# Kernel optimization log

Hardware: AMD Instinct MI355X
Metric: run time of the kernel (lower is better)

Reference implementation:

```python
import jax, jax.numpy as jnp
import numpy as np

NUM_TOKENS = 128
STRING_SIZE = 512
HIDDEN_SIZE = 2048
L_IN = 256
L_OUT = 256
MAX_PROGRAM_LENGTH = 10


def _lstm_scan(xs, h, c, Wih, Whh, b):
    """Run a PyTorch-convention LSTM (gate order i,f,g,o) over xs [L, D]."""
    def step(carry, x):
        h, c = carry
        g = x @ Wih.T + h @ Whh.T + b          # [4H]
        i, f, gg, o = jnp.split(g, 4)
        c2 = jax.nn.sigmoid(f) * c + jax.nn.sigmoid(i) * jnp.tanh(gg)
        h2 = jax.nn.sigmoid(o) * jnp.tanh(c2)
        return (h2, c2), None
    (h, c), _ = jax.lax.scan(step, (h, c), xs)
    return h, c


def setup_inputs() -> dict:
    key = jax.random.key(0)
    ks = jax.random.split(key, 13)
    H, S = HIDDEN_SIZE, STRING_SIZE
    def p(k, shape, scale=0.02):
        return scale * jax.random.normal(k, shape, dtype=jnp.float32)
    return {
        "input_sequence": jax.random.randint(ks[0], (L_IN,), 0, NUM_TOKENS),
        "output_sequence": jax.random.randint(ks[1], (L_OUT,), 0, NUM_TOKENS),
        "embed": p(ks[2], (NUM_TOKENS, S), 1.0),
        "eos": p(ks[3], (S,), 1.0),
        "in_Wih": p(ks[4], (4 * H, S)), "in_Whh": p(ks[5], (4 * H, H)), "in_b": p(ks[6], (4 * H,)),
        "out_Wih": p(ks[7], (4 * H, S)), "out_Whh": p(ks[8], (4 * H, H)), "out_b": p(ks[9], (4 * H,)),
        "prog_Wih": p(ks[10], (4 * H, H)), "prog_Whh": p(ks[11], (4 * H, H)), "prog_b": p(ks[12], (4 * H,)),
    }


def reference(input_sequence, output_sequence, embed, eos,
              in_Wih, in_Whh, in_b, out_Wih, out_Whh, out_b,
              prog_Wih, prog_Whh, prog_b):
    H = in_Whh.shape[1]
    h = jnp.zeros((H,), embed.dtype)
    c = jnp.zeros((H,), embed.dtype)
    # encode input string (+ end-of-sequence token) with input_lstm
    xs_in = jnp.concatenate([embed[input_sequence], eos[None]], axis=0)   # [L_in+1, S]
    h, c = _lstm_scan(xs_in, h, c, in_Wih, in_Whh, in_b)
    # encode output string (+ eos) with output_lstm, state carried over
    xs_out = jnp.concatenate([embed[output_sequence], eos[None]], axis=0)  # [L_out+1, S]
    h, c = _lstm_scan(xs_out, h, c, out_Wih, out_Whh, out_b)
    def prog_step(carry, _):
        h, c = carry
        g = h @ prog_Wih.T + h @ prog_Whh.T + prog_b
        i, f, gg, o = jnp.split(g, 4)
        c2 = jax.nn.sigmoid(f) * c + jax.nn.sigmoid(i) * jnp.tanh(gg)
        h2 = jax.nn.sigmoid(o) * jnp.tanh(c2)
        return (h2, c2), h2
    _, prog = jax.lax.scan(prog_step, (h, c), None, length=MAX_PROGRAM_LENGTH)
    return prog  # [MAX_PROGRAM_LENGTH, H] (stack of program hidden states)
```

## Files before the change

kernel.cpp:

```cpp
#include <hip/hip_runtime.h>

typedef unsigned short u16;
typedef unsigned int u32;
typedef unsigned long long u64;

#define NBLK 256

__device__ __forceinline__ float b2f(u16 u) {
    u32 i = ((u32)u) << 16;
    return __builtin_bit_cast(float, i);
}
__device__ __forceinline__ u16 f2b(float f) {
    u32 b = __builtin_bit_cast(u32, f);
    b += 0x7FFFu + ((b >> 16) & 1u);
    return (u16)(b >> 16);
}
__device__ __forceinline__ float sigm(float x) {
    return 1.f / (1.f + __expf(-x));
}
__device__ __forceinline__ float tanh_fast(float x) {
    float a = fabsf(x);
    float e = __expf(-2.f * a);
    float r = (1.f - e) / (1.f + e);
    return copysignf(r, x);
}

__global__ void __launch_bounds__(256)
xproj_kernel(const float* __restrict__ embed, const float* __restrict__ eos,
             const int* __restrict__ seq, const float* __restrict__ W,
             const float* __restrict__ bias, float* __restrict__ Xp)
{
    __shared__ float xs[8][512];
    const int tid = threadIdx.x;
    const int t0 = blockIdx.y * 8;
    const int nt = min(8, 257 - t0);

    for (int idx = tid; idx < nt * 512; idx += 256) {
        int tt = idx >> 9, col = idx & 511;
        int t = t0 + tt;
        xs[tt][col] = (t < 256) ? embed[(size_t)seq[t] * 512 + col] : eos[col];
    }
    __syncthreads();

    const int lane = tid & 63;
    const int wv = tid >> 6;

    float xr[8][8];
#pragma unroll
    for (int tt = 0; tt < 8; ++tt) {
        *(float4*)&xr[tt][0] = *(const float4*)&xs[tt][lane * 8];
        *(float4*)&xr[tt][4] = *(const float4*)&xs[tt][lane * 8 + 4];
    }

#pragma unroll 1
    for (int rr = 0; rr < 8; ++rr) {
        int r = blockIdx.x * 32 + wv * 8 + rr;
        float wf[8];
        *(float4*)&wf[0] = *(const float4*)&W[(size_t)r * 512 + lane * 8];
        *(float4*)&wf[4] = *(const float4*)&W[(size_t)r * 512 + lane * 8 + 4];
        float acc[8];
#pragma unroll
        for (int tt = 0; tt < 8; tt++) {
            float a = 0.f;
#pragma unroll
            for (int j = 0; j < 8; j++) a = fmaf(wf[j], xr[tt][j], a);
            acc[tt] = a;
        }
#pragma unroll
        for (int tt = 0; tt < 8; tt++) {
            float a = acc[tt];
#pragma unroll
            for (int off = 32; off > 0; off >>= 1) a += __shfl_xor(a, off, 64);
            if (lane == 0 && tt < nt) {
                int g = r >> 11, rem = r & 2047, wgi = rem >> 3, j = rem & 7;
                Xp[(size_t)(t0 + tt) * 8192 + (wgi << 5) + (g << 3) + j] = a + bias[r];
            }
        }
    }
}

__global__ void __launch_bounds__(512, 1)
rnn_coop(const float* __restrict__ WhhA, const float* __restrict__ WhhB,
         const float* __restrict__ pWih, const float* __restrict__ pWhh,
         const float* __restrict__ pB,
         const float* __restrict__ Xp0, const float* __restrict__ Xp1,
         u32* __restrict__ hseqB, float* __restrict__ out)
{
    __shared__ __align__(16) float hs[2048];
    __shared__ float gsum[32];

    const int wg = blockIdx.x;
    const int tid = threadIdx.x;
    const int lane = tid & 63;
    const int wv = tid >> 6;

    float w[4][32];
    float c_reg = 0.f;

    if (tid < 32) gsum[tid] = 0.f;

    float xp_cur = 0.f, xp_nxt = 0.f;
    if (wv == 0 && lane < 32)
        xp_cur = Xp0[(size_t)0 * 8192 + (wg << 5) + lane];

    for (int t = 0; t < 524; ++t) {
        const int phase = (t < 257) ? 0 : (t < 514) ? 1 : 2;

        if (t == 0 || t == 257 || t == 514) {
            if (phase < 2) {
                const float* Ws = phase ? WhhB : WhhA;
#pragma unroll
                for (int rr = 0; rr < 4; ++rr) {
                    int rl = (wv << 2) + rr;
                    const float* Wr = Ws + (size_t)(((rl >> 3) << 11) + (wg << 3) + (rl & 7)) * 2048;
#pragma unroll
                    for (int q = 0; q < 8; ++q)
                        *(float4*)&w[rr][q * 4] = *(const float4*)&Wr[(q << 8) + (lane << 2)];
                }
            } else {
#pragma unroll
                for (int rr = 0; rr < 4; ++rr) {
                    int rl = (wv << 2) + rr;
                    size_t off = (size_t)(((rl >> 3) << 11) + (wg << 3) + (rl & 7)) * 2048;
#pragma unroll
                    for (int q = 0; q < 8; ++q) {
                        float4 a = *(const float4*)&pWih[off + (q << 8) + (lane << 2)];
                        float4 b = *(const float4*)&pWhh[off + (q << 8) + (lane << 2)];
                        float4 s;
                        s.x = a.x + b.x; s.y = a.y + b.y;
                        s.z = a.z + b.z; s.w = a.w + b.w;
                        *(float4*)&w[rr][q * 4] = s;
                    }
                }
            }
        }

        if (t > 0) {
            const u64* src = (const u64*)hseqB + (size_t)(t - 1) * 512 + tid;
            u64 a = __hip_atomic_load(src, __ATOMIC_RELAXED, __HIP_MEMORY_SCOPE_AGENT);
            while ((u16)a == 0xFFFFu || (u16)(a >> 16) == 0xFFFFu ||
                   (u16)(a >> 32) == 0xFFFFu || (u16)(a >> 48) == 0xFFFFu) {
                __builtin_amdgcn_s_sleep(1);
                a = __hip_atomic_load(src, __ATOMIC_RELAXED, __HIP_MEMORY_SCOPE_AGENT);
            }
            float4 hv;
            hv.x = b2f((u16)a);         hv.y = b2f((u16)(a >> 16));
            hv.z = b2f((u16)(a >> 32)); hv.w = b2f((u16)(a >> 48));
            *(float4*)&hs[tid << 2] = hv;
        }
        __syncthreads();

        if (wv == 0 && lane < 32 && t < 523) {
            const int tn = t + 1;
            if (tn < 257)       xp_nxt = Xp0[(size_t)tn * 8192 + (wg << 5) + lane];
            else if (tn < 514)  xp_nxt = Xp1[(size_t)(tn - 257) * 8192 + (wg << 5) + lane];
            else                xp_nxt = pB[((lane >> 3) << 11) + (wg << 3) + (lane & 7)];
        }

        if (t > 0) {
            float a0 = 0.f, a1 = 0.f, a2 = 0.f, a3 = 0.f;
#pragma unroll
            for (int q = 0; q < 8; ++q) {
                float4 hv = *(const float4*)&hs[(q << 8) + (lane << 2)];
#pragma unroll
                for (int j = 0; j < 4; ++j) {
                    float h = ((const float*)&hv)[j];
                    a0 = fmaf(w[0][q * 4 + j], h, a0);
                    a1 = fmaf(w[1][q * 4 + j], h, a1);
                    a2 = fmaf(w[2][q * 4 + j], h, a2);
                    a3 = fmaf(w[3][q * 4 + j], h, a3);
                }
            }
#pragma unroll
            for (int off = 32; off > 0; off >>= 1) {
                a0 += __shfl_xor(a0, off, 64);
                a1 += __shfl_xor(a1, off, 64);
                a2 += __shfl_xor(a2, off, 64);
                a3 += __shfl_xor(a3, off, 64);
            }
            if (lane == 0) {
                const int rl = wv << 2;
                gsum[rl]     = a0;
                gsum[rl + 1] = a1;
                gsum[rl + 2] = a2;
                gsum[rl + 3] = a3;
            }
        }
        __syncthreads();

        if (wv == 0) {
            float tot = xp_cur + gsum[lane & 31];
            float act = ((lane >> 3) == 2) ? tanh_fast(tot) : sigm(tot);
            const int j = lane & 7;
            float fi = __shfl(act, j, 64);
            float ff = __shfl(act, 8 + j, 64);
            float fg = __shfl(act, 16 + j, 64);
            float fo = __shfl(act, 24 + j, 64);
            c_reg = ff * c_reg + fi * fg;
            float h2 = fo * tanh_fast(c_reg);
            u32 hb = (u32)f2b(h2);
            u32 lo = (u32)__shfl((int)hb, (lane & 3) * 2, 64);
            u32 hi = (u32)__shfl((int)hb, (lane & 3) * 2 + 1, 64);
            if (lane < 4)
                __hip_atomic_store(&hseqB[(size_t)t * 1024 + (wg << 2) + lane],
                                   (hi << 16) | lo,
                                   __ATOMIC_RELAXED, __HIP_MEMORY_SCOPE_AGENT);
            if (phase == 2 && lane < 8)
                out[(size_t)(t - 514) * 2048 + (wg << 3) + lane] = h2;
        }
        xp_cur = xp_nxt;
    }
}

extern "C" void kernel_launch(void* const* d_in, const int* in_sizes, int n_in,
                              void* d_out, int out_size, void* d_ws, size_t ws_size,
                              hipStream_t stream) {
    const int*   in_seq   = (const int*)d_in[0];
    const int*   out_seq  = (const int*)d_in[1];
    const float* embed    = (const float*)d_in[2];
    const float* eos      = (const float*)d_in[3];
    const float* in_Wih   = (const float*)d_in[4];
    const float* in_Whh   = (const float*)d_in[5];
    const float* in_b     = (const float*)d_in[6];
    const float* out_Wih  = (const float*)d_in[7];
    const float* out_Whh  = (const float*)d_in[8];
    const float* out_b    = (const float*)d_in[9];
    const float* pg_Wih   = (const float*)d_in[10];
    const float* pg_Whh   = (const float*)d_in[11];
    const float* pg_b     = (const float*)d_in[12];

    float* Xp0   = (float*)d_ws;
    float* Xp1   = Xp0 + (size_t)257 * 8192;
    u32*   hseqB = (u32*)(Xp1 + (size_t)257 * 8192);

    hipMemsetAsync(hseqB, 0xFF, (size_t)524 * 1024 * sizeof(u32), stream);

    dim3 g1(256, 33), b1(256);
    hipLaunchKernelGGL(xproj_kernel, g1, b1, 0, stream, embed, eos, in_seq,  in_Wih,  in_b,  Xp0);
    hipLaunchKernelGGL(xproj_kernel, g1, b1, 0, stream, embed, eos, out_seq, out_Wih, out_b, Xp1);

    float* out = (float*)d_out;
    void* args[] = { (void*)&in_Whh, (void*)&out_Whh, (void*)&pg_Wih, (void*)&pg_Whh,
                     (void*)&pg_b, (void*)&Xp0, (void*)&Xp1, (void*)&hseqB, (void*)&out };
    hipLaunchCooperativeKernel((const void*)rnn_coop, dim3(NBLK), dim3(512),
                               args, 0, stream);
}
```

Before: 1.984 ms.

## Fuse input projection into recurrent cooperative kernel with shared-memory Wih and lookahead ring

Removes the two separate xproj kernels and their global Xp buffers. Each workgroup now keeps its 32 rows of the input and output Wih in LDS and computes the input projection four steps ahead into a small ring buffer, so this work sits inside otherwise idle time in the serial recurrence. The token embedding for upcoming steps is prefetched into a double buffer. The s_sleep in the spin-wait is also removed, which should cut wake-up latency at the cost of more polling traffic. In exchange, each step adds extra LDS work and uses about 140KB of LDS per block.

New measurement: 2.274 ms. +14.6%, slower.

```diff
diff --git a/kernel.cpp b/kernel.cpp
--- a/kernel.cpp
+++ b/kernel.cpp
@@ -25,69 +25,22 @@
     return copysignf(r, x);
 }
 
-__global__ void __launch_bounds__(256)
-xproj_kernel(const float* __restrict__ embed, const float* __restrict__ eos,
-             const int* __restrict__ seq, const float* __restrict__ W,
-             const float* __restrict__ bias, float* __restrict__ Xp)
-{
-    __shared__ float xs[8][512];
-    const int tid = threadIdx.x;
-    const int t0 = blockIdx.y * 8;
-    const int nt = min(8, 257 - t0);
-
-    for (int idx = tid; idx < nt * 512; idx += 256) {
-        int tt = idx >> 9, col = idx & 511;
-        int t = t0 + tt;
-        xs[tt][col] = (t < 256) ? embed[(size_t)seq[t] * 512 + col] : eos[col];
-    }
-    __syncthreads();
-
-    const int lane = tid & 63;
-    const int wv = tid >> 6;
-
-    float xr[8][8];
-#pragma unroll
-    for (int tt = 0; tt < 8; ++tt) {
-        *(float4*)&xr[tt][0] = *(const float4*)&xs[tt][lane * 8];
-        *(float4*)&xr[tt][4] = *(const float4*)&xs[tt][lane * 8 + 4];
-    }
-
-#pragma unroll 1
-    for (int rr = 0; rr < 8; ++rr) {
-        int r = blockIdx.x * 32 + wv * 8 + rr;
-        float wf[8];
-        *(float4*)&wf[0] = *(const float4*)&W[(size_t)r * 512 + lane * 8];
-        *(float4*)&wf[4] = *(const float4*)&W[(size_t)r * 512 + lane * 8 + 4];
-        float acc[8];
-#pragma unroll
-        for (int tt = 0; tt < 8; tt++) {
-            float a = 0.f;
-#pragma unroll
-            for (int j = 0; j < 8; j++) a = fmaf(wf[j], xr[tt][j], a);
-            acc[tt] = a;
-        }
-#pragma unroll
-        for (int tt = 0; tt < 8; tt++) {
-            float a = acc[tt];
-#pragma unroll
-            for (int off = 32; off > 0; off >>= 1) a += __shfl_xor(a, off, 64);
-            if (lane == 0 && tt < nt) {
-                int g = r >> 11, rem = r & 2047, wgi = rem >> 3, j = rem & 7;
-                Xp[(size_t)(t0 + tt) * 8192 + (wgi << 5) + (g << 3) + j] = a + bias[r];
-            }
-        }
-    }
-}
-
 __global__ void __launch_bounds__(512, 1)
 rnn_coop(const float* __restrict__ WhhA, const float* __restrict__ WhhB,
          const float* __restrict__ pWih, const float* __restrict__ pWhh,
          const float* __restrict__ pB,
-         const float* __restrict__ Xp0, const float* __restrict__ Xp1,
+         const float* __restrict__ inWih, const float* __restrict__ outWih,
+         const float* __restrict__ in_b, const float* __restrict__ out_b,
+         const float* __restrict__ embed, const float* __restrict__ eos,
+         const int* __restrict__ in_seq, const int* __restrict__ out_seq,
          u32* __restrict__ hseqB, float* __restrict__ out)
 {
+    __shared__ __align__(16) float wihA[32 * 512];
+    __shared__ __align__(16) float wihB[32 * 512];
     __shared__ __align__(16) float hs[2048];
-    __shared__ float gsum[32];
+    __shared__ __align__(16) float xbuf[2][512];
+    __shared__ float ring[8][32];
+    __shared__ float biasA[32], biasB[32], gsum[32];
 
     const int wg = blockIdx.x;
     const int tid = threadIdx.x;
@@ -96,12 +49,57 @@
 
     float w[4][32];
     float c_reg = 0.f;
-
-    if (tid < 32) gsum[tid] = 0.f;
-
-    float xp_cur = 0.f, xp_nxt = 0.f;
-    if (wv == 0 && lane < 32)
-        xp_cur = Xp0[(size_t)0 * 8192 + (wg << 5) + lane];
+    float xp2 = 0.f;
+
+    for (int idx = tid; idx < 4096; idx += 512) {
+        int m = idx >> 7, c4 = (idx & 127) << 2;
+        size_t grow = (size_t)(((m >> 3) << 11) + (wg << 3) + (m & 7)) * 512;
+        *(float4*)&wihA[m * 512 + c4] = *(const float4*)&inWih[grow + c4];
+        *(float4*)&wihB[m * 512 + c4] = *(const float4*)&outWih[grow + c4];
+    }
+    if (tid < 32) {
+        int gofs = ((tid >> 3) << 11) + (wg << 3) + (tid & 7);
+        biasA[tid] = in_b[gofs];
+        biasB[tid] = out_b[gofs];
+        gsum[tid] = 0.f;
+    }
+    __syncthreads();
+
+    for (int tt = 0; tt < 4; ++tt) {
+        xbuf[0][tid] = embed[(size_t)in_seq[tt] * 512 + tid];
+        __syncthreads();
+        float a0 = 0.f, a1 = 0.f, a2 = 0.f, a3 = 0.f;
+        const int m0 = wv << 2;
+#pragma unroll
+        for (int q = 0; q < 2; ++q) {
+            float4 xv = *(const float4*)&xbuf[0][(q << 8) + (lane << 2)];
+            float4 w0 = *(const float4*)&wihA[(m0 + 0) * 512 + (q << 8) + (lane << 2)];
+            float4 w1 = *(const float4*)&wihA[(m0 + 1) * 512 + (q << 8) + (lane << 2)];
+            float4 w2 = *(const float4*)&wihA[(m0 + 2) * 512 + (q << 8) + (lane << 2)];
+            float4 w3 = *(const float4*)&wihA[(m0 + 3) * 512 + (q << 8) + (lane << 2)];
+            a0 = fmaf(w0.x, xv.x, fmaf(w0.y, xv.y, fmaf(w0.z, xv.z, fmaf(w0.w, xv.w, a0))));
+            a1 = fmaf(w1.x, xv.x, fmaf(w1.y, xv.y, fmaf(w1.z, xv.z, fmaf(w1.w, xv.w, a1))));
+            a2 = fmaf(w2.x, xv.x, fmaf(w2.y, xv.y, fmaf(w2.z, xv.z, fmaf(w2.w, xv.w, a2))));
+            a3 = fmaf(w3.x, xv.x, fmaf(w3.y, xv.y, fmaf(w3.z, xv.z, fmaf(w3.w, xv.w, a3))));
+        }
+#pragma unroll
+        for (int off = 32; off > 0; off >>= 1) {
+            a0 += __shfl_xor(a0, off, 64);
+            a1 += __shfl_xor(a1, off, 64);
+            a2 += __shfl_xor(a2, off, 64);
+            a3 += __shfl_xor(a3, off, 64);
+        }
+        if (lane == 0) {
+            ring[tt][m0]     = a0 + biasA[m0];
+            ring[tt][m0 + 1] = a1 + biasA[m0 + 1];
+            ring[tt][m0 + 2] = a2 + biasA[m0 + 2];
+            ring[tt][m0 + 3] = a3 + biasA[m0 + 3];
+        }
+        __syncthreads();
+    }
+    xbuf[0][tid] = embed[(size_t)in_seq[4] * 512 + tid];
+    int tok_cur = in_seq[5];
+    __syncthreads();
 
     for (int t = 0; t < 524; ++t) {
         const int phase = (t < 257) ? 0 : (t < 514) ? 1 : 2;
@@ -132,6 +130,8 @@
                         *(float4*)&w[rr][q * 4] = s;
                     }
                 }
+                if (wv == 0 && lane < 32)
+                    xp2 = pB[((lane >> 3) << 11) + (wg << 3) + (lane & 7)];
             }
         }
 
@@ -139,10 +139,8 @@
             const u64* src = (const u64*)hseqB + (size_t)(t - 1) * 512 + tid;
             u64 a = __hip_atomic_load(src, __ATOMIC_RELAXED, __HIP_MEMORY_SCOPE_AGENT);
             while ((u16)a == 0xFFFFu || (u16)(a >> 16) == 0xFFFFu ||
-                   (u16)(a >> 32) == 0xFFFFu || (u16)(a >> 48) == 0xFFFFu) {
-                __builtin_amdgcn_s_sleep(1);
+                   (u16)(a >> 32) == 0xFFFFu || (u16)(a >> 48) == 0xFFFFu)
                 a = __hip_atomic_load(src, __ATOMIC_RELAXED, __HIP_MEMORY_SCOPE_AGENT);
-            }
             float4 hv;
             hv.x = b2f((u16)a);         hv.y = b2f((u16)(a >> 16));
             hv.z = b2f((u16)(a >> 32)); hv.w = b2f((u16)(a >> 48));
@@ -150,12 +148,14 @@
         }
         __syncthreads();
 
-        if (wv == 0 && lane < 32 && t < 523) {
-            const int tn = t + 1;
-            if (tn < 257)       xp_nxt = Xp0[(size_t)tn * 8192 + (wg << 5) + lane];
-            else if (tn < 514)  xp_nxt = Xp1[(size_t)(tn - 257) * 8192 + (wg << 5) + lane];
-            else                xp_nxt = pB[((lane >> 3) << 11) + (wg << 3) + (lane & 7)];
-        }
+        const int idx1 = t + 5, idx2 = t + 6;
+        int tok_nxt = -2;
+        float xnext = 0.f;
+        if (idx2 <= 513)
+            tok_nxt = (idx2 < 257) ? ((idx2 < 256) ? in_seq[idx2] : -1)
+                                   : ((idx2 < 513) ? out_seq[idx2 - 257] : -1);
+        if (idx1 <= 513)
+            xnext = (tok_cur < 0) ? eos[tid] : embed[(size_t)tok_cur * 512 + tid];
 
         if (t > 0) {
             float a0 = 0.f, a1 = 0.f, a2 = 0.f, a3 = 0.f;
@@ -189,7 +189,8 @@
         __syncthreads();
 
         if (wv == 0) {
-            float tot = xp_cur + gsum[lane & 31];
+            float xpv = (phase < 2) ? ring[t & 7][lane & 31] : xp2;
+            float tot = xpv + gsum[lane & 31];
             float act = ((lane >> 3) == 2) ? tanh_fast(tot) : sigm(tot);
             const int j = lane & 7;
             float fi = __shfl(act, j, 64);
@@ -208,7 +209,43 @@
             if (phase == 2 && lane < 8)
                 out[(size_t)(t - 514) * 2048 + (wg << 3) + lane] = h2;
         }
-        xp_cur = xp_nxt;
+
+        const int tt = t + 4;
+        if (tt <= 513) {
+            const bool inph = tt < 257;
+            const float* wih = inph ? wihA : wihB;
+            const float* bl  = inph ? biasA : biasB;
+            const float* xb  = xbuf[tt & 1];
+            float a0 = 0.f, a1 = 0.f, a2 = 0.f, a3 = 0.f;
+            const int m0 = wv << 2;
+#pragma unroll
+            for (int q = 0; q < 2; ++q) {
+                float4 xv = *(const float4*)&xb[(q << 8) + (lane << 2)];
+                float4 w0 = *(const float4*)&wih[(m0 + 0) * 512 + (q << 8) + (lane << 2)];
+                float4 w1 = *(const float4*)&wih[(m0 + 1) * 512 + (q << 8) + (lane << 2)];
+                float4 w2 = *(const float4*)&wih[(m0 + 2) * 512 + (q << 8) + (lane << 2)];
+                float4 w3 = *(const float4*)&wih[(m0 + 3) * 512 + (q << 8) + (lane << 2)];
+                a0 = fmaf(w0.x, xv.x, fmaf(w0.y, xv.y, fmaf(w0.z, xv.z, fmaf(w0.w, xv.w, a0))));
+                a1 = fmaf(w1.x, xv.x, fmaf(w1.y, xv.y, fmaf(w1.z, xv.z, fmaf(w1.w, xv.w, a1))));
+                a2 = fmaf(w2.x, xv.x, fmaf(w2.y, xv.y, fmaf(w2.z, xv.z, fmaf(w2.w, xv.w, a2))));
+                a3 = fmaf(w3.x, xv.x, fmaf(w3.y, xv.y, fmaf(w3.z, xv.z, fmaf(w3.w, xv.w, a3))));
+            }
+#pragma unroll
+            for (int off = 32; off > 0; off >>= 1) {
+                a0 += __shfl_xor(a0, off, 64);
+                a1 += __shfl_xor(a1, off, 64);
+                a2 += __shfl_xor(a2, off, 64);
+                a3 += __shfl_xor(a3, off, 64);
+            }
+            if (lane == 0) {
+                ring[tt & 7][m0]     = a0 + bl[m0];
+                ring[tt & 7][m0 + 1] = a1 + bl[m0 + 1];
+                ring[tt & 7][m0 + 2] = a2 + bl[m0 + 2];
+                ring[tt & 7][m0 + 3] = a3 + bl[m0 + 3];
+            }
+        }
+        if (idx1 <= 513) xbuf[idx1 & 1][tid] = xnext;
+        tok_cur = tok_nxt;
     }
 }
 
@@ -229,19 +266,16 @@
     const float* pg_Whh   = (const float*)d_in[11];
     const float* pg_b     = (const float*)d_in[12];
 
-    float* Xp0   = (float*)d_ws;
-    float* Xp1   = Xp0 + (size_t)257 * 8192;
-    u32*   hseqB = (u32*)(Xp1 + (size_t)257 * 8192);
+    u32* hseqB = (u32*)d_ws;
 
     hipMemsetAsync(hseqB, 0xFF, (size_t)524 * 1024 * sizeof(u32), stream);
-
-    dim3 g1(256, 33), b1(256);
-    hipLaunchKernelGGL(xproj_kernel, g1, b1, 0, stream, embed, eos, in_seq,  in_Wih,  in_b,  Xp0);
-    hipLaunchKernelGGL(xproj_kernel, g1, b1, 0, stream, embed, eos, out_seq, out_Wih, out_b, Xp1);
 
     float* out = (float*)d_out;
     void* args[] = { (void*)&in_Whh, (void*)&out_Whh, (void*)&pg_Wih, (void*)&pg_Whh,
-                     (void*)&pg_b, (void*)&Xp0, (void*)&Xp1, (void*)&hseqB, (void*)&out };
+                     (void*)&pg_b,
+                     (void*)&in_Wih, (void*)&out_Wih, (void*)&in_b, (void*)&out_b,
+                     (void*)&embed, (void*)&eos, (void*)&in_seq, (void*)&out_seq,
+                     (void*)&hseqB, (void*)&out };
     hipLaunchCooperativeKernel((const void*)rnn_coop, dim3(NBLK), dim3(512),
                                args, 0, stream);
 }
```

## Merge input projections into one launch with weights held in registers

Applied to the files above, without the earlier changes.

The two xproj launches become a single 512-block launch, with blockIdx selecting the input or output LSTM. Each block now loads its 32 weight rows once into registers and loops over all 33 timestep groups, instead of re-reading weights for each (row, group) block. Shuffle reductions are batched across 8 rows to gain ILP. The cost is fewer blocks (512 versus 2×8448) and more registers per thread, which may lower occupancy. The recurrent kernel that dominates total time is unchanged.

Result: no change. 1.968 ms (-0.8%).

```diff
diff --git a/kernel.cpp b/kernel.cpp
--- a/kernel.cpp
+++ b/kernel.cpp
@@ -27,55 +27,73 @@
 
 __global__ void __launch_bounds__(256)
 xproj_kernel(const float* __restrict__ embed, const float* __restrict__ eos,
-             const int* __restrict__ seq, const float* __restrict__ W,
-             const float* __restrict__ bias, float* __restrict__ Xp)
+             const int* __restrict__ seqA, const int* __restrict__ seqB,
+             const float* __restrict__ WA, const float* __restrict__ WB,
+             const float* __restrict__ bA, const float* __restrict__ bB,
+             float* __restrict__ XpA, float* __restrict__ XpB)
 {
-    __shared__ float xs[8][512];
+    __shared__ __align__(16) float xs[8][512];
+    const int which = blockIdx.x >> 8;
+    const int bx = blockIdx.x & 255;
+    const int* __restrict__ seq  = which ? seqB : seqA;
+    const float* __restrict__ W  = which ? WB : WA;
+    const float* __restrict__ bias = which ? bB : bA;
+    float* __restrict__ Xp = which ? XpB : XpA;
+
     const int tid = threadIdx.x;
-    const int t0 = blockIdx.y * 8;
-    const int nt = min(8, 257 - t0);
-
-    for (int idx = tid; idx < nt * 512; idx += 256) {
-        int tt = idx >> 9, col = idx & 511;
-        int t = t0 + tt;
-        xs[tt][col] = (t < 256) ? embed[(size_t)seq[t] * 512 + col] : eos[col];
-    }
-    __syncthreads();
-
     const int lane = tid & 63;
     const int wv = tid >> 6;
 
-    float xr[8][8];
-#pragma unroll
-    for (int tt = 0; tt < 8; ++tt) {
-        *(float4*)&xr[tt][0] = *(const float4*)&xs[tt][lane * 8];
-        *(float4*)&xr[tt][4] = *(const float4*)&xs[tt][lane * 8 + 4];
+    float w[8][8];
+    float breg[8];
+    int slot[8];
+#pragma unroll
+    for (int rr = 0; rr < 8; ++rr) {
+        const int r = bx * 32 + wv * 8 + rr;
+        *(float4*)&w[rr][0] = *(const float4*)&W[(size_t)r * 512 + (lane << 2)];
+        *(float4*)&w[rr][4] = *(const float4*)&W[(size_t)r * 512 + 256 + (lane << 2)];
+        breg[rr] = bias[r];
+        int g = r >> 11, rem = r & 2047;
+        slot[rr] = ((rem >> 3) << 5) + (g << 3) + (rem & 7);
     }
 
+    for (int grp = 0; grp < 33; ++grp) {
+        const int t0 = grp * 8;
+        const int nt = min(8, 257 - t0);
+        for (int idx = tid; idx < nt * 512; idx += 256) {
+            int tt = idx >> 9, col = idx & 511;
+            int t = t0 + tt;
+            xs[tt][col] = (t < 256) ? embed[(size_t)seq[t] * 512 + col] : eos[col];
+        }
+        __syncthreads();
+
 #pragma unroll 1
-    for (int rr = 0; rr < 8; ++rr) {
-        int r = blockIdx.x * 32 + wv * 8 + rr;
-        float wf[8];
-        *(float4*)&wf[0] = *(const float4*)&W[(size_t)r * 512 + lane * 8];
-        *(float4*)&wf[4] = *(const float4*)&W[(size_t)r * 512 + lane * 8 + 4];
-        float acc[8];
-#pragma unroll
-        for (int tt = 0; tt < 8; tt++) {
-            float a = 0.f;
-#pragma unroll
-            for (int j = 0; j < 8; j++) a = fmaf(wf[j], xr[tt][j], a);
-            acc[tt] = a;
-        }
-#pragma unroll
-        for (int tt = 0; tt < 8; tt++) {
-            float a = acc[tt];
-#pragma unroll
-            for (int off = 32; off > 0; off >>= 1) a += __shfl_xor(a, off, 64);
+        for (int tt = 0; tt < 8; ++tt) {
+            float xt[8];
+            *(float4*)&xt[0] = *(const float4*)&xs[tt][(lane << 2)];
+            *(float4*)&xt[4] = *(const float4*)&xs[tt][256 + (lane << 2)];
+            float a[8];
+#pragma unroll
+            for (int rr = 0; rr < 8; ++rr) {
+                float s = 0.f;
+#pragma unroll
+                for (int j = 0; j < 8; ++j) s = fmaf(w[rr][j], xt[j], s);
+                a[rr] = s;
+            }
+#pragma unroll
+            for (int off = 32; off > 0; off >>= 1) {
+#pragma unroll
+                for (int rr = 0; rr < 8; ++rr)
+                    a[rr] += __shfl_xor(a[rr], off, 64);
+            }
             if (lane == 0 && tt < nt) {
-                int g = r >> 11, rem = r & 2047, wgi = rem >> 3, j = rem & 7;
-                Xp[(size_t)(t0 + tt) * 8192 + (wgi << 5) + (g << 3) + j] = a + bias[r];
-            }
-        }
+                float* dst = Xp + (size_t)(t0 + tt) * 8192;
+#pragma unroll
+                for (int rr = 0; rr < 8; ++rr)
+                    dst[slot[rr]] = a[rr] + breg[rr];
+            }
+        }
+        __syncthreads();
     }
 }
 
@@ -235,9 +253,9 @@
 
     hipMemsetAsync(hseqB, 0xFF, (size_t)524 * 1024 * sizeof(u32), stream);
 
-    dim3 g1(256, 33), b1(256);
-    hipLaunchKernelGGL(xproj_kernel, g1, b1, 0, stream, embed, eos, in_seq,  in_Wih,  in_b,  Xp0);
-    hipLaunchKernelGGL(xproj_kernel, g1, b1, 0, stream, embed, eos, out_seq, out_Wih, out_b, Xp1);
+    hipLaunchKernelGGL(xproj_kernel, dim3(512), dim3(256), 0, stream,
+                       embed, eos, in_seq, out_seq,
+                       in_Wih, out_Wih, in_b, out_b, Xp0, Xp1);
 
     float* out = (float*)d_out;
     void* args[] = { (void*)&in_Whh, (void*)&out_Whh, (void*)&pg_Wih, (void*)&pg_Whh,
```
